# Optimization experiments

Hardware: AMD Instinct MI355X
Metric: run time of the kernel (lower is better)

Reference implementation:

```python
import jax, jax.numpy as jnp
import numpy as np

NS, NV = 48, 10
N_NODES, N_EDGES = 10000, 100000
N_EDGE_FEAT = 3 * NS  # 144
W_SS, W_VS, W_SV, W_VV = NS * NS, NV * NS, NS * NV, NV * NV
W_NUMEL = W_SS + W_VS + W_SV + W_VV  # 3364 = FullyConnectedTensorProduct.weight_numel
IN_DIM = NS + 3 * NV  # 78
EPS = 1e-5


def setup_inputs() -> dict:
    key = jax.random.key(0)
    ks = jax.random.split(key, 8)
    return {
        "node_attr": jax.random.normal(ks[0], (N_NODES, IN_DIM), jnp.float32),
        "edge_attr": jax.random.normal(ks[1], (N_EDGES, N_EDGE_FEAT), jnp.float32),
        "edge_sh": jax.random.normal(ks[2], (N_EDGES, 4), jnp.float32),
        "fc1_w": jax.random.normal(ks[3], (N_EDGE_FEAT, N_EDGE_FEAT), jnp.float32) / np.sqrt(N_EDGE_FEAT).astype(np.float32),
        "fc1_b": jnp.zeros((N_EDGE_FEAT,), jnp.float32),
        "fc2_w": jax.random.normal(ks[4], (N_EDGE_FEAT, W_NUMEL), jnp.float32) / np.sqrt(N_EDGE_FEAT).astype(np.float32),
        "fc2_b": jnp.zeros((W_NUMEL,), jnp.float32),
        "bn_weight": jnp.ones((NS + NV,), jnp.float32),
        "bn_bias": jnp.zeros((NS,), jnp.float32),
        "edge_index": jax.random.randint(ks[5], (2, N_EDGES), 0, N_NODES),
    }


def reference(node_attr, edge_attr, edge_sh, fc1_w, fc1_b, fc2_w, fc2_b, bn_weight, bn_bias, edge_index):
    edge_src, edge_dst = edge_index[0], edge_index[1]
    # --- gather node feats per edge, split into irreps ---
    x = node_attr[edge_dst]                      # [E, 78]
    xs = x[:, :NS]                               # [E, 48]  scalars (0e)
    xv = x[:, NS:].reshape(-1, NV, 3)            # [E, 10, 3] vectors (1o)
    s0 = edge_sh[:, 0]                           # [E]     sh 0e
    s1 = edge_sh[:, 1:4]                         # [E, 3]  sh 1o

    # --- per-edge TP weights from edge MLP ---
    w = jax.nn.relu(edge_attr @ fc1_w + fc1_b) @ fc2_w + fc2_b  # [E, 3364]
    w_ss = w[:, :W_SS].reshape(-1, NS, NS)
    w_vs = w[:, W_SS:W_SS + W_VS].reshape(-1, NV, NS)
    w_sv = w[:, W_SS + W_VS:W_SS + W_VS + W_SV].reshape(-1, NS, NV)
    w_vv = w[:, W_SS + W_VS + W_SV:].reshape(-1, NV, NV)

    # path normalization: 1/sqrt(mul_in * n_paths_into_output_irrep)
    a_ss = 1.0 / np.sqrt(NS * 2.0)
    a_vs = 1.0 / np.sqrt(NV * 2.0)
    a_sv = 1.0 / np.sqrt(NS * 2.0)
    a_vv = 1.0 / np.sqrt(NV * 2.0)

    # --- Clebsch-Gordan tensor product (fully connected, per-edge weights) ---
    # 0e (x) 0e -> 0e
    out_s = a_ss * jnp.einsum('ei,eio->eo', xs, w_ss) * s0[:, None]
    # 1o (x) 1o -> 0e  (CG = delta/sqrt(3))
    dot = jnp.einsum('eic,ec->ei', xv, s1) / np.sqrt(3.0)
    out_s = out_s + a_vs * jnp.einsum('ei,eio->eo', dot, w_vs)
    # 0e (x) 1o -> 1o
    out_v = a_sv * jnp.einsum('ei,eio->eo', xs, w_sv)[:, :, None] * s1[:, None, :]
    # 1o (x) 0e -> 1o
    out_v = out_v + a_vv * jnp.einsum('eic,eio->eoc', xv, w_vv) * s0[:, None, None]

    tp = jnp.concatenate([out_s, out_v.reshape(-1, 3 * NV)], axis=1)  # [E, 78]

    # --- scatter-mean to nodes ---
    sums = jax.ops.segment_sum(tp, edge_src, num_segments=N_NODES)
    cnt = jax.ops.segment_sum(jnp.ones((tp.shape[0],), tp.dtype), edge_src, num_segments=N_NODES)
    out = sums / jnp.maximum(cnt, 1.0)[:, None]

    # --- residual (in_dim == out_dim -> pad is a no-op) ---
    out = out + node_attr

    # --- equivariant batch norm (e3nn-style, batch statistics) ---
    os = out[:, :NS]
    ov = out[:, NS:].reshape(-1, NV, 3)
    mu = os.mean(0)
    var = os.var(0)
    os = (os - mu) / jnp.sqrt(var + EPS) * bn_weight[:NS] + bn_bias
    fn = (ov ** 2).sum(-1).mean(0) / 3.0  # component-normalized mean squared norm per channel
    ov = ov / jnp.sqrt(fn + EPS)[None, :, None] * bn_weight[NS:][None, :, None]
    return jnp.concatenate([os, ov.reshape(-1, 3 * NV)], axis=1)
```

## Files before the change

kernel.cpp:

```cpp
#include <hip/hip_runtime.h>
#include <hip/hip_bf16.h>

#define NS   48
#define NV   10
#define NEF  144
#define WN   3364
#define IND  78
#define NE   100000
#define NN   10000
#define EPS  1e-5f
#define HP   144
#define EB   128

#define A_SS 0.10206207261596575f
#define A_VS 0.22360679774997896f
#define A_SV 0.10206207261596575f
#define A_VV 0.22360679774997896f
#define RS3  0.5773502691896258f

typedef __attribute__((ext_vector_type(8)))  short    short8;
typedef __attribute__((ext_vector_type(16))) float    f32x16;
typedef __attribute__((ext_vector_type(4)))  int      int4v;
typedef __attribute__((ext_vector_type(4)))  float    float4v;
typedef __attribute__((ext_vector_type(2)))  __fp16   fp16x2;
typedef __attribute__((ext_vector_type(8)))  _Float16 half8;

#define MFMAH(a,b,c) __builtin_amdgcn_mfma_f32_32x32x16_f16((a),(b),(c),0,0,0)

#define TP_F    0
#define OFFS_F  7810160
#define CUR_F   7820164
#define EL_F    7830164
#define PART_F  7930164
#define RAW_F   8320164
#define WSBF_F  8320324

#define OFF_W1  0
#define OFF_B1  23040
#define OFF_B2  468480
#define OFF_B3  561664
#define N_PREP  608256

__device__ __forceinline__ short toh(float v) {
    return __builtin_bit_cast(short, (_Float16)v);
}
__device__ __forceinline__ float fromh(short s) {
    return (float)__builtin_bit_cast(_Float16, s);
}
__device__ __forceinline__ unsigned pkh2(float a, float b) {
    fp16x2 h = __builtin_amdgcn_cvt_pkrtz(a, b);
    return __builtin_bit_cast(unsigned, h);
}
__device__ __forceinline__ float waveReduceSum(float v) {
    #pragma unroll
    for (int o = 32; o > 0; o >>= 1) v += __shfl_down(v, o, 64);
    return v;
}
__device__ __forceinline__ void gl_lds16(const short* g, short* l) {
    __builtin_amdgcn_global_load_lds(
        (const __attribute__((address_space(1))) unsigned int*)g,
        (__attribute__((address_space(3))) unsigned int*)l, 16, 0, 0);
}

__device__ __forceinline__ float prep_fetch(int idx, const float* __restrict__ fc1_w,
                                            const float* __restrict__ fc2_w,
                                            const float* __restrict__ b2)
{
    float v = 0.f;
    if (idx < OFF_B1) {
        int r = idx;
        int tile = r / 4608, rem = r % 4608;
        int ks = rem / 512, l = (rem % 512) / 8, j = rem % 8;
        int n = tile * 32 + (l & 31);
        int k = ks * 16 + ((l >> 5) << 3) + j;
        v = (n < 144) ? fc1_w[k * 144 + n] : 0.f;
    } else if (idx < OFF_B2) {
        int r = idx - OFF_B1;
        if (r < 442368) {
            int i = r / 9216, rem = r % 9216;
            int tile = rem / 4608; rem %= 4608;
            int ks = rem / 512, l = (rem % 512) / 8, j = rem % 8;
            int n = tile * 32 + (l & 31);
            int k = ks * 16 + ((l >> 5) << 3) + j;
            if (n < 48)      v = fc2_w[(size_t)k * WN + i * 48 + n];
            else if (n < 58) v = fc2_w[(size_t)k * WN + 2784 + i * 10 + (n - 48)];
        } else {
            int rb = r - 442368;
            int tile = rb / 1536, rem = rb % 1536;
            int ks = rem / 512, l = (rem % 512) / 8, j = rem % 8;
            int n = tile * 32 + (l & 31);
            int k = ks * 16 + ((l >> 5) << 3) + j;
            if (n < 48)      v = b2[k * 48 + n];
            else if (n < 58) v = b2[2784 + k * 10 + (n - 48)];
        }
    } else if (idx < OFF_B3) {
        int r = idx - OFF_B2;
        if (r < 92160) {
            int i = r / 9216, rem = r % 9216;
            int tile = rem / 4608; rem %= 4608;
            int ks = rem / 512, l = (rem % 512) / 8, j = rem % 8;
            int n = tile * 32 + (l & 31);
            int k = ks * 16 + ((l >> 5) << 3) + j;
            if (n < 48) v = fc2_w[(size_t)k * WN + 2304 + i * 48 + n];
        } else {
            int rb = r - 92160;
            int tile = rb / 512, rem = rb % 512;
            int l = rem / 8, j = rem % 8;
            int n = tile * 32 + (l & 31);
            int k = ((l >> 5) << 3) + j;
            if (k < 10 && n < 48) v = b2[2304 + k * 48 + n];
        }
    } else {
        int r = idx - OFF_B3;
        if (r < 46080) {
            int i = r / 4608, rem = r % 4608;
            int ks = rem / 512, l = (rem % 512) / 8, j = rem % 8;
            int n = l & 31;
            int k = ks * 16 + ((l >> 5) << 3) + j;
            if (n < 10) v = fc2_w[(size_t)k * WN + 3264 + i * 10 + n];
        } else {
            int rb = r - 46080;
            int l = rb / 8, j = rb % 8;
            int n = l & 31;
            int k = ((l >> 5) << 3) + j;
            if (k < 10 && n < 10) v = b2[3264 + k * 10 + n];
        }
    }
    return v;
}

__global__ void prep_weights(const float* __restrict__ fc1_w,
                             const float* __restrict__ fc2_w,
                             const float* __restrict__ b2,
                             short* __restrict__ wsbf)
{
    int tid = blockIdx.x * 256 + threadIdx.x;
    if (tid >= N_PREP / 8) return;
    int base = tid * 8;
    short8 outv;
    #pragma unroll
    for (int j = 0; j < 8; ++j)
        outv[j] = toh(prep_fetch(base + j, fc1_w, fc2_w, b2));
    *reinterpret_cast<short8*>(wsbf + base) = outv;
}

__global__ __launch_bounds__(1024) void histscan_kernel(const int* __restrict__ eidx,
                                                        int* __restrict__ offs,
                                                        int* __restrict__ cursor)
{
    __shared__ int cnt[NN];
    __shared__ int part[1024];
    int t = threadIdx.x;
    for (int i = t; i < NN; i += 1024) cnt[i] = 0;
    __syncthreads();
    for (int e = t; e < NE; e += 1024) atomicAdd(&cnt[eidx[e]], 1);
    __syncthreads();
    int base = t * 10;
    int local[10];
    int s = 0;
    #pragma unroll
    for (int q = 0; q < 10; ++q) {
        int i = base + q;
        int v = (i < NN) ? cnt[i] : 0;
        local[q] = s; s += v;
    }
    part[t] = s;
    __syncthreads();
    for (int o = 1; o < 1024; o <<= 1) {
        int v = (t >= o) ? part[t - o] : 0;
        __syncthreads();
        part[t] += v;
        __syncthreads();
    }
    int prev = (t == 0) ? 0 : part[t - 1];
    #pragma unroll
    for (int q = 0; q < 10; ++q) {
        int i = base + q;
        if (i < NN) { int val = prev + local[q]; offs[i] = val; cursor[i] = val; }
    }
    if (t == 1023) offs[NN] = part[1023];
}

__global__ void scatter_kernel(const int* __restrict__ eidx,
                               int* __restrict__ cursor, int* __restrict__ elist)
{
    int e = blockIdx.x * 256 + threadIdx.x;
    if (e < NE) {
        int pos = atomicAdd(&cursor[eidx[e]], 1);
        elist[pos] = e;
    }
}

__global__ __launch_bounds__(256, 2) void fused_main(
    const float* __restrict__ node_attr, const float* __restrict__ edge_attr,
    const float* __restrict__ edge_sh,   const float* __restrict__ b1,
    const int*   __restrict__ eidx,      const short* __restrict__ wsbf,
    short* __restrict__ tp)
{
    __shared__ short ubuf[18432];
    __shared__ short xfT[96 * EB];
    __shared__ float pbuf[EB][10];
    __shared__ float s0s[EB];
    __shared__ float s1s[EB][3];

    const int t    = threadIdx.x;
    const int e0   = blockIdx.x * EB;
    const int lane = t & 63, wave = t >> 6;
    const int n32  = lane & 31, kh = lane >> 5;
    const int eL   = 32 * wave + n32;
    const int eLc  = min(e0 + eL, NE - 1);

    const short* W1L = wsbf + OFF_W1 + lane * 8;
    const short* B1L = wsbf + OFF_B1 + lane * 8;
    const short* B2L = wsbf + OFF_B2 + lane * 8;
    const short* B3L = wsbf + OFF_B3 + lane * 8;

    auto stageB = [&](const short* src, short* dst, int nfrag) {
        for (int f = wave; f < nfrag; f += 4)
            gl_lds16(src + f * 512 + lane * 8, dst + f * 512);
    };

    for (int idx = t; idx < 8 * EB; idx += 256) xfT[88 * EB + idx] = 0;

    if (t < EB) {
        int ee = e0 + t;
        if (ee < NE) {
            float4v sh = *reinterpret_cast<const float4v*>(edge_sh + (size_t)ee * 4);
            s0s[t] = sh.x; s1s[t][0] = sh.y; s1s[t][1] = sh.z; s1s[t][2] = sh.w;
        } else {
            s0s[t] = 0.f; s1s[t][0] = s1s[t][1] = s1s[t][2] = 0.f;
        }
    }

    {
        const int eg  = t & (EB - 1);
        const int jb  = t >> 7;
        const int egc = min(e0 + eg, NE - 1);
        const int dst = eidx[NE + egc];
        const float* na = node_attr + (size_t)dst * IND;
        for (int j = jb; j < IND; j += 2) {
            int slot = (j < NS) ? j : 58 + ((j - NS) % 3) * 10 + (j - NS) / 3;
            xfT[slot * EB + eg] = toh(na[j]);
        }
    }

    half8 afc[9];
    {
        const float* ea = edge_attr + (size_t)eLc * NEF + kh * 8;
        #pragma unroll
        for (int ks = 0; ks < 9; ++ks) {
            float4v lo = *reinterpret_cast<const float4v*>(ea + ks * 16);
            float4v hi = *reinterpret_cast<const float4v*>(ea + ks * 16 + 4);
            int4v v = { (int)pkh2(lo.x, lo.y), (int)pkh2(lo.z, lo.w),
                        (int)pkh2(hi.x, hi.y), (int)pkh2(hi.z, hi.w) };
            afc[ks] = __builtin_bit_cast(half8, v);
        }
    }
    __syncthreads();

    #pragma unroll
    for (int it = 0; it < 5; ++it) {
        int e = t & (EB - 1);
        int i = (t >> 7) + 2 * it;
        float d = fromh(xfT[(58 + i) * EB + e]) * s1s[e][0]
                + fromh(xfT[(68 + i) * EB + e]) * s1s[e][1]
                + fromh(xfT[(78 + i) * EB + e]) * s1s[e][2];
        xfT[(48 + i) * EB + e] = toh(d * RS3);
    }

    for (int pass = 0; pass < 3; ++pass) {
        int ntA = 2 * pass, ntB = 2 * pass + 1;
        bool hasB = (pass < 2);
        f32x16 accA = 0, accB = 0;
        #pragma unroll
        for (int ks = 0; ks < 9; ++ks) {
            half8 bA = *(const half8*)(W1L + (ntA * 9 + ks) * 512);
            accA = MFMAH(afc[ks], bA, accA);
            if (hasB) {
                half8 bB = *(const half8*)(W1L + (ntB * 9 + ks) * 512);
                accB = MFMAH(afc[ks], bB, accB);
            }
        }
        int colA = ntA * 32 + n32, colB = ntB * 32 + n32;
        float b1A = (colA < NEF) ? b1[colA] : 0.f;
        float b1B = (hasB && colB < NEF) ? b1[colB] : 0.f;
        #pragma unroll
        for (int r = 0; r < 16; ++r) {
            int row = (r & 3) + 8 * (r >> 2) + 4 * kh;
            int e = 32 * wave + row;
            if (colA < NEF) ubuf[e * HP + colA] = toh(fmaxf(accA[r] + b1A, 0.f));
            if (hasB)       ubuf[e * HP + colB] = toh(fmaxf(accB[r] + b1B, 0.f));
        }
    }

    half8 hh[9];
    #pragma unroll
    for (int ks = 0; ks < 9; ++ks)
        hh[ks] = *(const half8*)(ubuf + eL * HP + ks * 16 + kh * 8);
    __syncthreads();

    short* stg0 = ubuf;
    short* stg1 = ubuf + 9216;

    stageB(wsbf + OFF_B1, stg0, 18);
    __syncthreads();

    auto splat8 = [&](int slot) -> half8 {
        _Float16 xh = __builtin_bit_cast(_Float16, xfT[slot * EB + eL]);
        half8 r = { xh, xh, xh, xh, xh, xh, xh, xh };
        return r;
    };

    f32x16 acc1a = 0, acc1b = 0, acc2a = 0, acc2b = 0;
    {
        #pragma unroll 1
        for (int i = 0; i < 48; ++i) {
            short* cur = (i & 1) ? stg1 : stg0;
            short* nxt = (i & 1) ? stg0 : stg1;
            if (i < 47) stageB(wsbf + OFF_B1 + (i + 1) * 9216, nxt, 18);
            else        stageB(wsbf + OFF_B2, nxt, 18);
            half8 x8 = splat8(i);
            #pragma unroll
            for (int ks = 0; ks < 9; ++ks) {
                half8 a  = hh[ks] * x8;
                half8 b0 = *(const half8*)(cur + ks * 512 + lane * 8);
                half8 b1f= *(const half8*)(cur + 4608 + ks * 512 + lane * 8);
                acc1a = MFMAH(a, b0, acc1a);
                acc1b = MFMAH(a, b1f, acc1b);
            }
            __syncthreads();
        }
        #pragma unroll
        for (int ks = 0; ks < 3; ++ks) {
            short8 a;
            #pragma unroll
            for (int j = 0; j < 8; ++j)
                a[j] = xfT[(ks * 16 + kh * 8 + j) * EB + eL];
            half8 ah = __builtin_bit_cast(half8, a);
            half8 b0 = *(const half8*)(B1L + 442368 + ks * 512);
            half8 b1f= *(const half8*)(B1L + 442368 + 1536 + ks * 512);
            acc1a = MFMAH(ah, b0, acc1a);
            acc1b = MFMAH(ah, b1f, acc1b);
        }
    }
    {
        #pragma unroll 1
        for (int i = 0; i < 10; ++i) {
            short* cur = (i & 1) ? stg1 : stg0;
            short* nxt = (i & 1) ? stg0 : stg1;
            if (i < 9) stageB(wsbf + OFF_B2 + (i + 1) * 9216, nxt, 18);
            else       stageB(wsbf + OFF_B3, nxt, 9);
            half8 x8 = splat8(48 + i);
            #pragma unroll
            for (int ks = 0; ks < 9; ++ks) {
                half8 a  = hh[ks] * x8;
                half8 b0 = *(const half8*)(cur + ks * 512 + lane * 8);
                half8 b1f= *(const half8*)(cur + 4608 + ks * 512 + lane * 8);
                acc2a = MFMAH(a, b0, acc2a);
                acc2b = MFMAH(a, b1f, acc2b);
            }
            __syncthreads();
        }
        {
            short8 a;
            #pragma unroll
            for (int j = 0; j < 8; ++j)
                a[j] = xfT[(48 + kh * 8 + j) * EB + eL];
            half8 ah = __builtin_bit_cast(half8, a);
            half8 b0 = *(const half8*)(B2L + 92160);
            half8 b1f= *(const half8*)(B2L + 92160 + 512);
            acc2a = MFMAH(ah, b0, acc2a);
            acc2b = MFMAH(ah, b1f, acc2b);
        }
    }
    #pragma unroll
    for (int r = 0; r < 16; ++r) {
        int row = (r & 3) + 8 * (r >> 2) + 4 * kh;
        int e = 32 * wave + row;
        int ge = e0 + e;
        if (ge < NE) {
            float s0e = s0s[e];
            short* rowp = tp + (size_t)ge * IND;
            rowp[n32] = toh(A_SS * s0e * acc1a[r] + A_VS * acc2a[r]);
            int col = 32 + n32;
            if (col < 48) {
                rowp[col] = toh(A_SS * s0e * acc1b[r] + A_VS * acc2b[r]);
            } else if (col < 58) {
                pbuf[e][col - 48] = A_SV * acc1b[r];
            }
        }
    }
    {
        f32x16 acc30 = 0, acc31 = 0, acc32 = 0;
        #pragma unroll 1
        for (int i = 0; i < 10; ++i) {
            short* cur = (i & 1) ? stg1 : stg0;
            short* nxt = (i & 1) ? stg0 : stg1;
            if (i < 9) stageB(wsbf + OFF_B3 + (i + 1) * 4608, nxt, 9);
            half8 x0 = splat8(58 + i), x1 = splat8(68 + i), x2 = splat8(78 + i);
            #pragma unroll
            for (int ks = 0; ks < 9; ++ks) {
                half8 b0 = *(const half8*)(cur + ks * 512 + lane * 8);
                acc30 = MFMAH(hh[ks] * x0, b0, acc30);
                acc31 = MFMAH(hh[ks] * x1, b0, acc31);
                acc32 = MFMAH(hh[ks] * x2, b0, acc32);
            }
            __syncthreads();
        }
        {
            half8 bb = *(const half8*)(B3L + 46080);
            short8 a;
            #pragma unroll
            for (int j = 0; j < 8; ++j) a[j] = xfT[(58 + kh * 8 + j) * EB + eL];
            acc30 = MFMAH(__builtin_bit_cast(half8, a), bb, acc30);
            #pragma unroll
            for (int j = 0; j < 8; ++j) a[j] = xfT[(68 + kh * 8 + j) * EB + eL];
            acc31 = MFMAH(__builtin_bit_cast(half8, a), bb, acc31);
            #pragma unroll
            for (int j = 0; j < 8; ++j) a[j] = xfT[(78 + kh * 8 + j) * EB + eL];
            acc32 = MFMAH(__builtin_bit_cast(half8, a), bb, acc32);
        }
        if (n32 < 10) {
            #pragma unroll
            for (int r = 0; r < 16; ++r) {
                int row = (r & 3) + 8 * (r >> 2) + 4 * kh;
                int e = 32 * wave + row;
                int ge = e0 + e;
                if (ge < NE) {
                    float p  = pbuf[e][n32];
                    float qs = A_VV * s0s[e];
                    size_t base = (size_t)ge * IND + 48 + n32 * 3;
                    tp[base + 0] = toh(p * s1s[e][0] + qs * acc30[r]);
                    tp[base + 1] = toh(p * s1s[e][1] + qs * acc31[r]);
                    tp[base + 2] = toh(p * s1s[e][2] + qs * acc32[r]);
                }
            }
        }
    }
}

__global__ __launch_bounds__(256) void gather_kernel(const short* __restrict__ tp,
                                                     const int* __restrict__ offs,
                                                     const int* __restrict__ elist,
                                                     const float* __restrict__ node_attr,
                                                     float* __restrict__ out,
                                                     float* __restrict__ partial)
{
    __shared__ float sS[IND], sQ[IND];
    int t = threadIdx.x;
    if (t < IND) { sS[t] = 0.f; sQ[t] = 0.f; }
    __syncthreads();

    int node = blockIdx.x * 4 + (t >> 6);
    int lane = t & 63;
    int beg = offs[node], end = offs[node + 1];
    float a0 = 0.f, a1 = 0.f;
    for (int p = beg; p < end; ++p) {
        int e = elist[p];
        const short* row = tp + (size_t)e * IND;
        a0 += fromh(row[lane]);
        if (lane < 14) a1 += fromh(row[64 + lane]);
    }
    float c = fmaxf((float)(end - beg), 1.0f);
    size_t base = (size_t)node * IND;
    float v0 = a0 / c + node_attr[base + lane];
    out[base + lane] = v0;
    atomicAdd(&sS[lane], v0);
    atomicAdd(&sQ[lane], v0 * v0);
    if (lane < 14) {
        float v1 = a1 / c + node_attr[base + 64 + lane];
        out[base + 64 + lane] = v1;
        atomicAdd(&sS[64 + lane], v1);
        atomicAdd(&sQ[64 + lane], v1 * v1);
    }
    __syncthreads();
    if (t < IND)            partial[(size_t)t * 2500 + blockIdx.x] = sS[t];
    else if (t < 2 * IND)   partial[(size_t)(t - IND + IND) * 2500 + blockIdx.x] = sQ[t - IND];
}

__global__ __launch_bounds__(256) void reduce_kernel(const float* __restrict__ partial,
                                                     float* __restrict__ raw)
{
    int f = blockIdx.x;
    float s = 0.f;
    for (int b = threadIdx.x; b < 2500; b += 256)
        s += partial[(size_t)f * 2500 + b];
    s = waveReduceSum(s);
    __shared__ float r[4];
    int w = threadIdx.x >> 6, lane = threadIdx.x & 63;
    if (lane == 0) r[w] = s;
    __syncthreads();
    if (threadIdx.x == 0) raw[f] = r[0] + r[1] + r[2] + r[3];
}

__global__ void normalize_kernel(const float* __restrict__ raw,
                                 const float* __restrict__ bnw,
                                 const float* __restrict__ bnb,
                                 float* __restrict__ out)
{
    int idx = blockIdx.x * 256 + threadIdx.x;
    if (idx >= NN * IND) return;
    int j = idx % IND;
    float x = out[idx];
    const float inv = 1.0f / (float)NN;
    if (j < NS) {
        float mu  = raw[j] * inv;
        float var = raw[IND + j] * inv - mu * mu;
        out[idx] = (x - mu) * rsqrtf(var + EPS) * bnw[j] + bnb[j];
    } else {
        int v = (j - NS) / 3;
        float fn = (raw[IND + NS + 3 * v] + raw[IND + NS + 3 * v + 1] +
                    raw[IND + NS + 3 * v + 2]) * (inv / 3.0f);
        out[idx] = x * bnw[NS + v] * rsqrtf(fn + EPS);
    }
}

extern "C" void kernel_launch(void* const* d_in, const int* in_sizes, int n_in,
                              void* d_out, int out_size, void* d_ws, size_t ws_size,
                              hipStream_t stream)
{
    (void)in_sizes; (void)n_in; (void)out_size; (void)ws_size;
    const float* node_attr = (const float*)d_in[0];
    const float* edge_attr = (const float*)d_in[1];
    const float* edge_sh   = (const float*)d_in[2];
    const float* fc1_w     = (const float*)d_in[3];
    const float* fc1_b     = (const float*)d_in[4];
    const float* fc2_w     = (const float*)d_in[5];
    const float* fc2_b     = (const float*)d_in[6];
    const float* bn_w      = (const float*)d_in[7];
    const float* bn_b      = (const float*)d_in[8];
    const int*   eidx      = (const int*)d_in[9];

    float* wsf   = (float*)d_ws;
    short* tp    = (short*)(wsf + TP_F);
    int*   offs  = (int*)(wsf + OFFS_F);
    int*   cur   = (int*)(wsf + CUR_F);
    int*   elist = (int*)(wsf + EL_F);
    float* part  = wsf + PART_F;
    float* raw   = wsf + RAW_F;
    short* wsbf  = (short*)(wsf + WSBF_F);
    float* out   = (float*)d_out;

    prep_weights<<<(N_PREP / 8 + 255) / 256, 256, 0, stream>>>(fc1_w, fc2_w, fc2_b, wsbf);
    histscan_kernel<<<1, 1024, 0, stream>>>(eidx, offs, cur);
    scatter_kernel<<<(NE + 255) / 256, 256, 0, stream>>>(eidx, cur, elist);
    fused_main<<<(NE + EB - 1) / EB, 256, 0, stream>>>(node_attr, edge_attr, edge_sh,
                                                       fc1_b, eidx, wsbf, tp);
    gather_kernel<<<NN / 4, 256, 0, stream>>>(tp, offs, elist, node_attr, out, part);
    reduce_kernel<<<156, 256, 0, stream>>>(part, raw);
    normalize_kernel<<<(NN * IND + 255) / 256, 256, 0, stream>>>(raw, bn_w, bn_b, out);
}
```

Before: 339.8 us.

## Write TP rows in source-sorted order and parallelize histogram

The main kernel now writes each edge's tensor-product row to its position in the source-sorted order, via a per-edge position array built by the scatter kernel. The gather kernel can then read contiguous rows without an edge-list indirection. The single-block histogram is split into a grid-wide global-atomic histogram plus a memset and a separate scan kernel, which removes the serial one-block pass over all edges. In exchange, the main kernel's stores become scattered and there is one extra kernel launch plus a memset.

Result: faster. 324.6 us (-4.5%).

```diff
diff --git a/kernel.cpp b/kernel.cpp
--- a/kernel.cpp
+++ b/kernel.cpp
@@ -28,9 +28,10 @@
 #define MFMAH(a,b,c) __builtin_amdgcn_mfma_f32_32x32x16_f16((a),(b),(c),0,0,0)
 
 #define TP_F    0
+#define CNT_F   7800160
 #define OFFS_F  7810160
 #define CUR_F   7820164
-#define EL_F    7830164
+#define EPOS_F  7830164
 #define PART_F  7930164
 #define RAW_F   8320164
 #define WSBF_F  8320324
@@ -144,24 +145,25 @@
     *reinterpret_cast<short8*>(wsbf + base) = outv;
 }
 
-__global__ __launch_bounds__(1024) void histscan_kernel(const int* __restrict__ eidx,
-                                                        int* __restrict__ offs,
-                                                        int* __restrict__ cursor)
-{
-    __shared__ int cnt[NN];
+__global__ void hist_kernel(const int* __restrict__ eidx, int* __restrict__ cntI)
+{
+    int e = blockIdx.x * 256 + threadIdx.x;
+    if (e < NE) atomicAdd(&cntI[eidx[e]], 1);
+}
+
+__global__ __launch_bounds__(1024) void scan_kernel(const int* __restrict__ cntI,
+                                                    int* __restrict__ offs,
+                                                    int* __restrict__ cursor)
+{
     __shared__ int part[1024];
     int t = threadIdx.x;
-    for (int i = t; i < NN; i += 1024) cnt[i] = 0;
-    __syncthreads();
-    for (int e = t; e < NE; e += 1024) atomicAdd(&cnt[eidx[e]], 1);
-    __syncthreads();
     int base = t * 10;
     int local[10];
     int s = 0;
     #pragma unroll
     for (int q = 0; q < 10; ++q) {
         int i = base + q;
-        int v = (i < NN) ? cnt[i] : 0;
+        int v = (i < NN) ? cntI[i] : 0;
         local[q] = s; s += v;
     }
     part[t] = s;
@@ -182,26 +184,24 @@
 }
 
 __global__ void scatter_kernel(const int* __restrict__ eidx,
-                               int* __restrict__ cursor, int* __restrict__ elist)
+                               int* __restrict__ cursor, int* __restrict__ epos)
 {
     int e = blockIdx.x * 256 + threadIdx.x;
-    if (e < NE) {
-        int pos = atomicAdd(&cursor[eidx[e]], 1);
-        elist[pos] = e;
-    }
+    if (e < NE) epos[e] = atomicAdd(&cursor[eidx[e]], 1);
 }
 
 __global__ __launch_bounds__(256, 2) void fused_main(
     const float* __restrict__ node_attr, const float* __restrict__ edge_attr,
     const float* __restrict__ edge_sh,   const float* __restrict__ b1,
-    const int*   __restrict__ eidx,      const short* __restrict__ wsbf,
-    short* __restrict__ tp)
+    const int*   __restrict__ eidx,      const int* __restrict__ epos,
+    const short* __restrict__ wsbf,      short* __restrict__ tp)
 {
     __shared__ short ubuf[18432];
     __shared__ short xfT[96 * EB];
     __shared__ float pbuf[EB][10];
     __shared__ float s0s[EB];
     __shared__ float s1s[EB][3];
+    __shared__ int   eposs[EB];
 
     const int t    = threadIdx.x;
     const int e0   = blockIdx.x * EB;
@@ -227,8 +227,10 @@
         if (ee < NE) {
             float4v sh = *reinterpret_cast<const float4v*>(edge_sh + (size_t)ee * 4);
             s0s[t] = sh.x; s1s[t][0] = sh.y; s1s[t][1] = sh.z; s1s[t][2] = sh.w;
+            eposs[t] = epos[ee];
         } else {
             s0s[t] = 0.f; s1s[t][0] = s1s[t][1] = s1s[t][2] = 0.f;
+            eposs[t] = 0;
         }
     }
 
@@ -380,7 +382,7 @@
         int ge = e0 + e;
         if (ge < NE) {
             float s0e = s0s[e];
-            short* rowp = tp + (size_t)ge * IND;
+            short* rowp = tp + (size_t)eposs[e] * IND;
             rowp[n32] = toh(A_SS * s0e * acc1a[r] + A_VS * acc2a[r]);
             int col = 32 + n32;
             if (col < 48) {
@@ -429,7 +431,7 @@
                 if (ge < NE) {
                     float p  = pbuf[e][n32];
                     float qs = A_VV * s0s[e];
-                    size_t base = (size_t)ge * IND + 48 + n32 * 3;
+                    size_t base = (size_t)eposs[e] * IND + 48 + n32 * 3;
                     tp[base + 0] = toh(p * s1s[e][0] + qs * acc30[r]);
                     tp[base + 1] = toh(p * s1s[e][1] + qs * acc31[r]);
                     tp[base + 2] = toh(p * s1s[e][2] + qs * acc32[r]);
@@ -441,7 +443,6 @@
 
 __global__ __launch_bounds__(256) void gather_kernel(const short* __restrict__ tp,
                                                      const int* __restrict__ offs,
-                                                     const int* __restrict__ elist,
                                                      const float* __restrict__ node_attr,
                                                      float* __restrict__ out,
                                                      float* __restrict__ partial)
@@ -456,8 +457,7 @@
     int beg = offs[node], end = offs[node + 1];
     float a0 = 0.f, a1 = 0.f;
     for (int p = beg; p < end; ++p) {
-        int e = elist[p];
-        const short* row = tp + (size_t)e * IND;
+        const short* row = tp + (size_t)p * IND;
         a0 += fromh(row[lane]);
         if (lane < 14) a1 += fromh(row[64 + lane]);
     }
@@ -475,7 +475,7 @@
     }
     __syncthreads();
     if (t < IND)            partial[(size_t)t * 2500 + blockIdx.x] = sS[t];
-    else if (t < 2 * IND)   partial[(size_t)(t - IND + IND) * 2500 + blockIdx.x] = sQ[t - IND];
+    else if (t < 2 * IND)   partial[(size_t)(t) * 2500 + blockIdx.x] = sQ[t - IND];
 }
 
 __global__ __launch_bounds__(256) void reduce_kernel(const float* __restrict__ partial,
@@ -533,20 +533,23 @@
 
     float* wsf   = (float*)d_ws;
     short* tp    = (short*)(wsf + TP_F);
+    int*   cntI  = (int*)(wsf + CNT_F);
     int*   offs  = (int*)(wsf + OFFS_F);
     int*   cur   = (int*)(wsf + CUR_F);
-    int*   elist = (int*)(wsf + EL_F);
+    int*   epos  = (int*)(wsf + EPOS_F);
     float* part  = wsf + PART_F;
     float* raw   = wsf + RAW_F;
     short* wsbf  = (short*)(wsf + WSBF_F);
     float* out   = (float*)d_out;
 
+    (void)hipMemsetAsync(cntI, 0, NN * sizeof(int), stream);
     prep_weights<<<(N_PREP / 8 + 255) / 256, 256, 0, stream>>>(fc1_w, fc2_w, fc2_b, wsbf);
-    histscan_kernel<<<1, 1024, 0, stream>>>(eidx, offs, cur);
-    scatter_kernel<<<(NE + 255) / 256, 256, 0, stream>>>(eidx, cur, elist);
+    hist_kernel<<<(NE + 255) / 256, 256, 0, stream>>>(eidx, cntI);
+    scan_kernel<<<1, 1024, 0, stream>>>(cntI, offs, cur);
+    scatter_kernel<<<(NE + 255) / 256, 256, 0, stream>>>(eidx, cur, epos);
     fused_main<<<(NE + EB - 1) / EB, 256, 0, stream>>>(node_attr, edge_attr, edge_sh,
-                                                       fc1_b, eidx, wsbf, tp);
-    gather_kernel<<<NN / 4, 256, 0, stream>>>(tp, offs, elist, node_attr, out, part);
+                                                       fc1_b, eidx, epos, wsbf, tp);
+    gather_kernel<<<NN / 4, 256, 0, stream>>>(tp, offs, node_attr, out, part);
     reduce_kernel<<<156, 256, 0, stream>>>(part, raw);
     normalize_kernel<<<(NN * IND + 255) / 256, 256, 0, stream>>>(raw, bn_w, bn_b, out);
 }
```
